# Optimization experiments

Measured on AMD Instinct MI355X. Metric: run time of the kernel, lower is better.

Reference implementation:

```python
import jax, jax.numpy as jnp
import numpy as np

D_MODEL = 1024
N_HEADS = 16
HEAD_DIM = D_MODEL // N_HEADS  # 64
LATENT = 256
B, S = 2, 2048


def setup_inputs() -> dict:
    key = jax.random.key(0)
    ks = jax.random.split(key, 13)
    sc = 0.02
    inp = {
        'x': jax.random.normal(ks[0], (B, S, D_MODEL), jnp.float32),
        'Wq': jax.random.normal(ks[1], (D_MODEL, D_MODEL), jnp.float32) * sc,
        'bq': jnp.zeros((D_MODEL,), jnp.float32),
        'Wkd': jax.random.normal(ks[2], (D_MODEL, LATENT), jnp.float32) * sc,
        'bkd': jnp.zeros((LATENT,), jnp.float32),
        'Wvd': jax.random.normal(ks[3], (D_MODEL, LATENT), jnp.float32) * sc,
        'bvd': jnp.zeros((LATENT,), jnp.float32),
        'Wku': jax.random.normal(ks[4], (LATENT, D_MODEL), jnp.float32) * sc,
        'bku': jnp.zeros((D_MODEL,), jnp.float32),
        'Wvu': jax.random.normal(ks[5], (LATENT, D_MODEL), jnp.float32) * sc,
        'bvu': jnp.zeros((D_MODEL,), jnp.float32),
        'Wo': jax.random.normal(ks[6], (D_MODEL, D_MODEL), jnp.float32) * sc,
        'bo': jnp.zeros((D_MODEL,), jnp.float32),
    }
    return inp


def reference(x, Wq, bq, Wkd, bkd, Wvd, bvd, Wku, bku, Wvu, bvu, Wo, bo):
    b, s, _ = x.shape
    # projections
    Q = x @ Wq + bq                      # [b, s, d_model]
    K_latent = x @ Wkd + bkd             # [b, s, latent]
    V_latent = x @ Wvd + bvd             # [b, s, latent]
    K = K_latent @ Wku + bku             # [b, s, d_model]
    V = V_latent @ Wvu + bvu             # [b, s, d_model]
    # split heads
    Qh = Q.reshape(b, s, N_HEADS, HEAD_DIM)
    Kh = K.reshape(b, s, N_HEADS, HEAD_DIM)
    Vh = V.reshape(b, s, N_HEADS, HEAD_DIM)
    scale = 1.0 / jnp.sqrt(jnp.asarray(HEAD_DIM, x.dtype))
    scores = jnp.einsum('bqhd,bkhd->bhqk', Qh, Kh) * scale  # [b,h,s,s]
    attn = jax.nn.softmax(scores, axis=-1)
    ctx = jnp.einsum('bhqk,bkhd->bqhd', attn, Vh).reshape(b, s, D_MODEL)
    out = ctx @ Wo + bo
    return out
```

## Files before the change

### kernel.cpp

```cpp
#include <hip/hip_runtime.h>
#include <hip/hip_bf16.h>
#include <cstddef>

#define B_SZ 2
#define SEQ  2048
#define DM   1024
#define NH   16
#define HD   64
#define LAT  256
#define MTOT (B_SZ*SEQ)
#define NQKV 1536
#define QSCALE 0.18033688011112042f

typedef short bf16x8 __attribute__((ext_vector_type(8)));
typedef float floatx4 __attribute__((ext_vector_type(4)));
typedef unsigned short u16;

#if __has_builtin(__builtin_amdgcn_exp2f)
#define EXP2(x) __builtin_amdgcn_exp2f(x)
#else
#define EXP2(x) exp2f(x)
#endif

__device__ __forceinline__ u16 f2bf(float f) {
  union { float f; unsigned u; } a; a.f = f;
  unsigned r = a.u + 0x7FFFu + ((a.u >> 16) & 1u);
  return (u16)(r >> 16);
}

__device__ __forceinline__ floatx4 mfma16(bf16x8 a, bf16x8 b, floatx4 c) {
  return __builtin_amdgcn_mfma_f32_16x16x32_bf16(a, b, c, 0, 0, 0);
}

__device__ __forceinline__ void load16(const u16* g, u16* l) {
  __builtin_amdgcn_global_load_lds((const __attribute__((address_space(1))) unsigned*)g,
                                   (__attribute__((address_space(3))) unsigned*)l, 16, 0, 0);
}

__device__ void transpose_tile(const float* __restrict__ W, u16* __restrict__ WT,
                               int K, int N, int k0, int n0, u16 (*t)[65]) {
  const int r = threadIdx.x >> 4;
  const int c4 = (threadIdx.x & 15) * 4;
#pragma unroll
  for (int s = 0; s < 4; s++) {
    int row = s * 16 + r;
    float4 v = *(const float4*)&W[(size_t)(k0 + row) * N + n0 + c4];
    t[row][c4 + 0] = f2bf(v.x); t[row][c4 + 1] = f2bf(v.y);
    t[row][c4 + 2] = f2bf(v.z); t[row][c4 + 3] = f2bf(v.w);
  }
  __syncthreads();
  const int r2 = threadIdx.x >> 2;
  const int c8 = (threadIdx.x & 3) * 16;
  __align__(16) u16 tmp[16];
#pragma unroll
  for (int i = 0; i < 16; i++) tmp[i] = t[c8 + i][r2];
  u16* dst = WT + (size_t)(n0 + r2) * K + k0 + c8;
  *(bf16x8*)dst       = *(const bf16x8*)&tmp[0];
  *(bf16x8*)(dst + 8) = *(const bf16x8*)&tmp[8];
}

__global__ __launch_bounds__(256)
void prep_k(const float* __restrict__ x, u16* __restrict__ xb,
            const float* __restrict__ Wq, const float* __restrict__ Wkd,
            const float* __restrict__ Wvd, const float* __restrict__ Wku,
            const float* __restrict__ Wvu, const float* __restrict__ Wo,
            u16* __restrict__ WstkT, u16* __restrict__ WkuT,
            u16* __restrict__ WvuT, u16* __restrict__ WoT,
            const float* __restrict__ bq, const float* __restrict__ bkd,
            const float* __restrict__ bvd, float* __restrict__ bqkv) {
  __shared__ u16 t[64][65];
  const int blk = blockIdx.x;
  if (blk < 4096) {
    int i = blk * 256 + threadIdx.x;
    float4 v = ((const float4*)x)[i];
    ushort4 o; o.x = f2bf(v.x); o.y = f2bf(v.y); o.z = f2bf(v.z); o.w = f2bf(v.w);
    ((ushort4*)xb)[i] = o;
  } else if (blk < 4352) {
    int tt = blk - 4096;
    transpose_tile(Wq, WstkT, DM, DM, (tt >> 4) * 64, (tt & 15) * 64, t);
  } else if (blk < 4416) {
    int tt = blk - 4352;
    transpose_tile(Wkd, WstkT + (size_t)DM * DM, DM, LAT, (tt >> 2) * 64, (tt & 3) * 64, t);
  } else if (blk < 4480) {
    int tt = blk - 4416;
    transpose_tile(Wvd, WstkT + (size_t)1280 * DM, DM, LAT, (tt >> 2) * 64, (tt & 3) * 64, t);
  } else if (blk < 4544) {
    int tt = blk - 4480;
    transpose_tile(Wku, WkuT, LAT, DM, (tt >> 4) * 64, (tt & 15) * 64, t);
  } else if (blk < 4608) {
    int tt = blk - 4544;
    transpose_tile(Wvu, WvuT, LAT, DM, (tt >> 4) * 64, (tt & 15) * 64, t);
  } else if (blk < 4864) {
    int tt = blk - 4608;
    transpose_tile(Wo, WoT, DM, DM, (tt >> 4) * 64, (tt & 15) * 64, t);
  } else {
    int i = (blk - 4864) * 256 + threadIdx.x;
    float v = (i < 1024) ? bq[i] : (i < 1280) ? bkd[i - 1024] : bvd[i - 1280];
    bqkv[i] = v;
  }
}

template<int TM, int OUT_BF16, int VT1>
__global__ __launch_bounds__(256)
void gemm_bt(const u16* __restrict__ A0, const u16* __restrict__ A1,
             const u16* __restrict__ BT0, const u16* __restrict__ BT1,
             const float* __restrict__ bias0, const float* __restrict__ bias1,
             void* __restrict__ C0, void* __restrict__ C1,
             int M, int N, int Kd, int lda, float qscale, int qcols) {
  constexpr int FM = TM / 32;
  __shared__ u16 As[TM * 64];
  __shared__ u16 Bs[64 * 64];
  const u16* A  = blockIdx.z ? A1 : A0;
  const u16* BT = blockIdx.z ? BT1 : BT0;
  const float* bias = blockIdx.z ? bias1 : bias0;
  void* C = blockIdx.z ? C1 : C0;

  const int tid = threadIdx.x;
  const int m0 = blockIdx.y * TM, n0 = blockIdx.x * 64;
  const int wave = tid >> 6, lane = tid & 63;
  const int l15 = lane & 15, quad = lane >> 4;
  const int wm = (wave >> 1) * (TM / 2), wn = (wave & 1) * 32;

  floatx4 acc[FM][2];
#pragma unroll
  for (int i = 0; i < FM; i++)
#pragma unroll
    for (int j = 0; j < 2; j++) acc[i][j] = (floatx4){0.f, 0.f, 0.f, 0.f};

  const int tr = tid >> 3;
  const int tc8 = (tid & 7) * 8;
  const u16* Ag = A  + (size_t)(m0 + tr) * lda + tc8;
  const u16* Bg = BT + (size_t)(n0 + tr) * Kd + tc8;
  u16* AsW = &As[(size_t)tid * 8];
  u16* BsW = &Bs[(size_t)tid * 8];

  for (int k0 = 0; k0 < Kd; k0 += 64) {
    __syncthreads();
#pragma unroll
    for (int s = 0; s < FM; s++)
      load16(Ag + (size_t)(s * 32) * lda + k0, AsW + s * 2048);
#pragma unroll
    for (int s = 0; s < 2; s++)
      load16(Bg + (size_t)(s * 32) * Kd  + k0, BsW + s * 2048);
    __syncthreads();
#pragma unroll
    for (int kk = 0; kk < 2; kk++) {
      bf16x8 af[FM], bfr[2];
#pragma unroll
      for (int i = 0; i < FM; i++)
        af[i]  = *(const bf16x8*)&As[(wm + i * 16 + l15) * 64 + kk * 32 + quad * 8];
#pragma unroll
      for (int j = 0; j < 2; j++)
        bfr[j] = *(const bf16x8*)&Bs[(wn + j * 16 + l15) * 64 + kk * 32 + quad * 8];
#pragma unroll
      for (int i = 0; i < FM; i++)
#pragma unroll
        for (int j = 0; j < 2; j++)
          acc[i][j] = mfma16(af[i], bfr[j], acc[i][j]);
    }
  }

  if (VT1 && blockIdx.z == 1) {
#pragma unroll
    for (int i = 0; i < FM; i++) {
      int row = m0 + wm + i * 16 + quad * 4;
      int bb = row >> 11, sb = row & 2047;
#pragma unroll
      for (int j = 0; j < 2; j++) {
        int col = n0 + wn + j * 16 + l15;
        float bv = bias[col];
        union { u16 u[4]; uint2 w2; } tv;
#pragma unroll
        for (int r = 0; r < 4; r++) tv.u[r] = f2bf(acc[i][j][r] + bv);
        *(uint2*)((u16*)C + ((size_t)(bb * 16 + (col >> 6)) * 64 + (col & 63)) * SEQ + sb) = tv.w2;
      }
    }
  } else {
#pragma unroll
    for (int i = 0; i < FM; i++) {
      int row = m0 + wm + i * 16 + quad * 4;
#pragma unroll
      for (int j = 0; j < 2; j++) {
        int col = n0 + wn + j * 16 + l15;
        float bv = bias[col];
        float sc = (col < qcols) ? qscale : 1.f;
#pragma unroll
        for (int r = 0; r < 4; r++) {
          float v = (acc[i][j][r] + bv) * sc;
          if (OUT_BF16) ((u16*)C)[(size_t)(row + r) * N + col] = f2bf(v);
          else          ((float*)C)[(size_t)(row + r) * N + col] = v;
        }
      }
    }
  }
}

__global__ __launch_bounds__(256, 2)
void attn_fused(const u16* __restrict__ Q, const u16* __restrict__ K,
                const u16* __restrict__ VT, u16* __restrict__ CTX) {
  __shared__ float Ocmb[64][68];
  __shared__ float Lw[4][64];
  __shared__ u16 Plds[4][64][40];
  const int bh = blockIdx.y, b = bh >> 4, h = bh & 15;
  const int wave = threadIdx.x >> 6, lane = threadIdx.x & 63;
  const int l15 = lane & 15, quad = lane >> 4;
  const int q0 = blockIdx.x * 64;

  bf16x8 qf[4][2];
  {
    const u16* Qp = Q + (size_t)(b * SEQ + q0 + l15) * NQKV + h * HD + quad * 8;
#pragma unroll
    for (int qi = 0; qi < 4; qi++)
#pragma unroll
      for (int h2 = 0; h2 < 2; h2++)
        qf[qi][h2] = *(const bf16x8*)(Qp + (size_t)qi * 16 * NQKV + h2 * 32);
  }
  const u16* Kp = K + (size_t)(b * SEQ) * DM + h * HD + quad * 8;
  const u16* Vp = VT + ((size_t)bh * HD + l15) * SEQ + quad * 8;

  floatx4 o[4][4];
#pragma unroll
  for (int dt = 0; dt < 4; dt++)
#pragma unroll
    for (int qi = 0; qi < 4; qi++) o[dt][qi] = (floatx4){0.f, 0.f, 0.f, 0.f};
  float ls[4] = {0.f, 0.f, 0.f, 0.f};

  const int kb0 = wave * 512;

  bf16x8 kfb[2][2][2], vfb[2][4];
#pragma unroll
  for (int ki = 0; ki < 2; ki++)
#pragma unroll
    for (int h2 = 0; h2 < 2; h2++)
      kfb[0][ki][h2] = *(const bf16x8*)(Kp + (size_t)(kb0 + ki * 16 + l15) * DM + h2 * 32);
#pragma unroll
  for (int dt = 0; dt < 4; dt++)
    vfb[0][dt] = *(const bf16x8*)(Vp + (size_t)(dt * 16) * SEQ + kb0);

#pragma unroll 2
  for (int it = 0; it < 16; ++it) {
    const int cur = it & 1, nxt = cur ^ 1;
    const int kb = kb0 + it * 32;
    if (it < 15) {
      const int kn = kb + 32;
#pragma unroll
      for (int ki = 0; ki < 2; ki++)
#pragma unroll
        for (int h2 = 0; h2 < 2; h2++)
          kfb[nxt][ki][h2] = *(const bf16x8*)(Kp + (size_t)(kn + ki * 16 + l15) * DM + h2 * 32);
#pragma unroll
      for (int dt = 0; dt < 4; dt++)
        vfb[nxt][dt] = *(const bf16x8*)(Vp + (size_t)(dt * 16) * SEQ + kn);
    }
    unsigned pw[4][4];
#pragma unroll
    for (int qi = 0; qi < 4; qi++) {
#pragma unroll
      for (int ki = 0; ki < 2; ki++) {
        floatx4 z = (floatx4){0.f, 0.f, 0.f, 0.f};
        z = mfma16(kfb[cur][ki][0], qf[qi][0], z);
        z = mfma16(kfb[cur][ki][1], qf[qi][1], z);
        float p0 = EXP2(z[0]), p1 = EXP2(z[1]), p2 = EXP2(z[2]), p3 = EXP2(z[3]);
        ls[qi] += (p0 + p1) + (p2 + p3);
        unsigned u0 = __float_as_uint(p0) + 0x8000u;
        unsigned u1 = __float_as_uint(p1) + 0x8000u;
        unsigned u2 = __float_as_uint(p2) + 0x8000u;
        unsigned u3 = __float_as_uint(p3) + 0x8000u;
        pw[qi][ki * 2]     = __builtin_amdgcn_perm(u1, u0, 0x07060302u);
        pw[qi][ki * 2 + 1] = __builtin_amdgcn_perm(u3, u2, 0x07060302u);
      }
    }
#pragma unroll
    for (int qi = 0; qi < 4; qi++) {
      uint2 w0; w0.x = pw[qi][0]; w0.y = pw[qi][1];
      *(uint2*)&Plds[wave][qi * 16 + l15][quad * 4] = w0;
      uint2 w1; w1.x = pw[qi][2]; w1.y = pw[qi][3];
      *(uint2*)&Plds[wave][qi * 16 + l15][16 + quad * 4] = w1;
    }
#pragma unroll
    for (int qi = 0; qi < 4; qi++) {
      bf16x8 pf = *(const bf16x8*)&Plds[wave][qi * 16 + l15][quad * 8];
#pragma unroll
      for (int dt = 0; dt < 4; dt++)
        o[dt][qi] = mfma16(vfb[cur][dt], pf, o[dt][qi]);
    }
  }

#pragma unroll
  for (int qi = 0; qi < 4; qi++) {
    float v = ls[qi];
    v += __shfl_xor(v, 16);
    v += __shfl_xor(v, 32);
    if (quad == 0) Lw[wave][qi * 16 + l15] = v;
  }
  if (wave == 0) {
#pragma unroll
    for (int dt = 0; dt < 4; dt++)
#pragma unroll
      for (int qi = 0; qi < 4; qi++)
        *(floatx4*)&Ocmb[qi * 16 + l15][dt * 16 + quad * 4] = o[dt][qi];
  }
  __syncthreads();
  if (wave == 1) {
#pragma unroll
    for (int dt = 0; dt < 4; dt++)
#pragma unroll
      for (int qi = 0; qi < 4; qi++) {
        floatx4* pp = (floatx4*)&Ocmb[qi * 16 + l15][dt * 16 + quad * 4];
        *pp = *pp + o[dt][qi];
      }
  }
  __syncthreads();
  if (wave == 2) {
#pragma unroll
    for (int dt = 0; dt < 4; dt++)
#pragma unroll
      for (int qi = 0; qi < 4; qi++) {
        floatx4* pp = (floatx4*)&Ocmb[qi * 16 + l15][dt * 16 + quad * 4];
        *pp = *pp + o[dt][qi];
      }
  }
  __syncthreads();
  if (wave == 3) {
#pragma unroll
    for (int qi = 0; qi < 4; qi++) {
      int qq = qi * 16 + l15;
      float lt = Lw[0][qq] + Lw[1][qq] + Lw[2][qq] + Lw[3][qq];
      float inv = 1.f / lt;
      u16* Crow = CTX + (size_t)(b * SEQ + q0 + qq) * DM + h * HD + quad * 4;
#pragma unroll
      for (int dt = 0; dt < 4; dt++) {
        floatx4 ov = o[dt][qi] + *(const floatx4*)&Ocmb[qq][dt * 16 + quad * 4];
        union { u16 u[4]; uint2 w2; } tv;
#pragma unroll
        for (int r = 0; r < 4; r++) tv.u[r] = f2bf(ov[r] * inv);
        *(uint2*)(Crow + dt * 16) = tv.w2;
      }
    }
  }
}

extern "C" void kernel_launch(void* const* d_in, const int* in_sizes, int n_in,
                              void* d_out, int out_size, void* d_ws, size_t ws_size,
                              hipStream_t stream) {
  const float* x   = (const float*)d_in[0];
  const float* Wq  = (const float*)d_in[1];
  const float* bq  = (const float*)d_in[2];
  const float* Wkd = (const float*)d_in[3];
  const float* bkd = (const float*)d_in[4];
  const float* Wvd = (const float*)d_in[5];
  const float* bvd = (const float*)d_in[6];
  const float* Wku = (const float*)d_in[7];
  const float* bku = (const float*)d_in[8];
  const float* Wvu = (const float*)d_in[9];
  const float* bvu = (const float*)d_in[10];
  const float* Wo  = (const float*)d_in[11];
  const float* bo  = (const float*)d_in[12];
  float* out = (float*)d_out;

  float* bqkv = (float*)d_ws;
  u16* p = (u16*)((char*)d_ws + 1536 * sizeof(float));
  u16* xb    = p; p += (size_t)MTOT * DM;
  u16* WstkT = p; p += (size_t)NQKV * DM;
  u16* WkuT  = p; p += (size_t)DM * LAT;
  u16* WvuT  = p; p += (size_t)DM * LAT;
  u16* WoT   = p; p += (size_t)DM * DM;
  u16* QKVb  = p; p += (size_t)MTOT * NQKV;
  u16* Kb    = p; p += (size_t)MTOT * DM;
  u16* VTb   = p; p += (size_t)MTOT * DM;
  u16* CXb   = p; p += (size_t)MTOT * DM;

  prep_k<<<4870, 256, 0, stream>>>(x, xb, Wq, Wkd, Wvd, Wku, Wvu, Wo,
                                   WstkT, WkuT, WvuT, WoT, bq, bkd, bvd, bqkv);

  gemm_bt<128, 1, 0><<<dim3(NQKV / 64, MTOT / 128, 1), 256, 0, stream>>>(
      xb, xb, WstkT, WstkT, bqkv, bqkv, QKVb, QKVb, MTOT, NQKV, DM, DM, QSCALE, DM);
  gemm_bt<128, 1, 1><<<dim3(DM / 64, MTOT / 128, 2), 256, 0, stream>>>(
      QKVb + 1024, QKVb + 1280, WkuT, WvuT, bku, bvu, Kb, VTb, MTOT, DM, LAT, NQKV, 1.f, 0);

  attn_fused<<<dim3(SEQ / 64, B_SZ * NH), 256, 0, stream>>>(QKVb, Kb, VTb, CXb);

  gemm_bt<64, 0, 0><<<dim3(DM / 64, MTOT / 64, 1), 256, 0, stream>>>(
      CXb, CXb, WoT, WoT, bo, bo, out, out, MTOT, DM, DM, DM, 1.f, 0);
}
```

Baseline: 223.3 us.

## Split attention waves 2x2 over query and key halves, drop prefetch buffers

Attention waves now split as two query halves times two key halves. Each wave handles 32 queries over 1024 keys, where before each wave took all 64 queries over 512 keys. The cross-wave reduction shrinks from a three-stage serialized LDS accumulate to one exchange. The register double-buffered K/V prefetch is removed and launch bounds are raised to 3 blocks per CU to gain occupancy instead. The output GEMM also moves to a 128-row tile. Each wave now issues K/V loads per query tile with less reuse and without software prefetch, which may expose memory latency.

```diff
diff --git a/kernel.cpp b/kernel.cpp
--- a/kernel.cpp
+++ b/kernel.cpp
@@ -195,22 +195,23 @@
   }
 }
 
-__global__ __launch_bounds__(256, 2)
+__global__ __launch_bounds__(256, 3)
 void attn_fused(const u16* __restrict__ Q, const u16* __restrict__ K,
                 const u16* __restrict__ VT, u16* __restrict__ CTX) {
-  __shared__ float Ocmb[64][68];
-  __shared__ float Lw[4][64];
-  __shared__ u16 Plds[4][64][40];
+  __shared__ float Ocmb[2][32][68];
+  __shared__ float Lw[2][32];
+  __shared__ u16 Plds[4][32][40];
   const int bh = blockIdx.y, b = bh >> 4, h = bh & 15;
   const int wave = threadIdx.x >> 6, lane = threadIdx.x & 63;
   const int l15 = lane & 15, quad = lane >> 4;
-  const int q0 = blockIdx.x * 64;
-
-  bf16x8 qf[4][2];
+  const int wq = wave & 1, wk = wave >> 1;
+  const int q0 = blockIdx.x * 64 + wq * 32;
+
+  bf16x8 qf[2][2];
   {
     const u16* Qp = Q + (size_t)(b * SEQ + q0 + l15) * NQKV + h * HD + quad * 8;
 #pragma unroll
-    for (int qi = 0; qi < 4; qi++)
+    for (int qi = 0; qi < 2; qi++)
 #pragma unroll
       for (int h2 = 0; h2 < 2; h2++)
         qf[qi][h2] = *(const bf16x8*)(Qp + (size_t)qi * 16 * NQKV + h2 * 32);
@@ -218,48 +219,36 @@
   const u16* Kp = K + (size_t)(b * SEQ) * DM + h * HD + quad * 8;
   const u16* Vp = VT + ((size_t)bh * HD + l15) * SEQ + quad * 8;
 
-  floatx4 o[4][4];
+  floatx4 o[4][2];
 #pragma unroll
   for (int dt = 0; dt < 4; dt++)
 #pragma unroll
-    for (int qi = 0; qi < 4; qi++) o[dt][qi] = (floatx4){0.f, 0.f, 0.f, 0.f};
-  float ls[4] = {0.f, 0.f, 0.f, 0.f};
-
-  const int kb0 = wave * 512;
-
-  bf16x8 kfb[2][2][2], vfb[2][4];
-#pragma unroll
-  for (int ki = 0; ki < 2; ki++)
-#pragma unroll
-    for (int h2 = 0; h2 < 2; h2++)
-      kfb[0][ki][h2] = *(const bf16x8*)(Kp + (size_t)(kb0 + ki * 16 + l15) * DM + h2 * 32);
-#pragma unroll
-  for (int dt = 0; dt < 4; dt++)
-    vfb[0][dt] = *(const bf16x8*)(Vp + (size_t)(dt * 16) * SEQ + kb0);
-
-#pragma unroll 2
-  for (int it = 0; it < 16; ++it) {
-    const int cur = it & 1, nxt = cur ^ 1;
+    for (int qi = 0; qi < 2; qi++) o[dt][qi] = (floatx4){0.f, 0.f, 0.f, 0.f};
+  float ls[2] = {0.f, 0.f};
+
+  const int kb0 = wk * 1024;
+
+  for (int it = 0; it < 32; ++it) {
     const int kb = kb0 + it * 32;
-    if (it < 15) {
-      const int kn = kb + 32;
-#pragma unroll
-      for (int ki = 0; ki < 2; ki++)
-#pragma unroll
-        for (int h2 = 0; h2 < 2; h2++)
-          kfb[nxt][ki][h2] = *(const bf16x8*)(Kp + (size_t)(kn + ki * 16 + l15) * DM + h2 * 32);
-#pragma unroll
-      for (int dt = 0; dt < 4; dt++)
-        vfb[nxt][dt] = *(const bf16x8*)(Vp + (size_t)(dt * 16) * SEQ + kn);
-    }
-    unsigned pw[4][4];
-#pragma unroll
-    for (int qi = 0; qi < 4; qi++) {
+    bf16x8 kf[2][2];
+#pragma unroll
+    for (int ki = 0; ki < 2; ki++)
+#pragma unroll
+      for (int h2 = 0; h2 < 2; h2++)
+        kf[ki][h2] = *(const bf16x8*)(Kp + (size_t)(kb + ki * 16 + l15) * DM + h2 * 32);
+    bf16x8 vf[4];
+#pragma unroll
+    for (int dt = 0; dt < 4; dt++)
+      vf[dt] = *(const bf16x8*)(Vp + (size_t)(dt * 16) * SEQ + kb);
+
+    unsigned pw[2][4];
+#pragma unroll
+    for (int qi = 0; qi < 2; qi++) {
 #pragma unroll
       for (int ki = 0; ki < 2; ki++) {
         floatx4 z = (floatx4){0.f, 0.f, 0.f, 0.f};
-        z = mfma16(kfb[cur][ki][0], qf[qi][0], z);
-        z = mfma16(kfb[cur][ki][1], qf[qi][1], z);
+        z = mfma16(kf[ki][0], qf[qi][0], z);
+        z = mfma16(kf[ki][1], qf[qi][1], z);
         float p0 = EXP2(z[0]), p1 = EXP2(z[1]), p2 = EXP2(z[2]), p3 = EXP2(z[3]);
         ls[qi] += (p0 + p1) + (p2 + p3);
         unsigned u0 = __float_as_uint(p0) + 0x8000u;
@@ -271,66 +260,49 @@
       }
     }
 #pragma unroll
-    for (int qi = 0; qi < 4; qi++) {
+    for (int qi = 0; qi < 2; qi++) {
       uint2 w0; w0.x = pw[qi][0]; w0.y = pw[qi][1];
       *(uint2*)&Plds[wave][qi * 16 + l15][quad * 4] = w0;
       uint2 w1; w1.x = pw[qi][2]; w1.y = pw[qi][3];
       *(uint2*)&Plds[wave][qi * 16 + l15][16 + quad * 4] = w1;
     }
 #pragma unroll
-    for (int qi = 0; qi < 4; qi++) {
+    for (int qi = 0; qi < 2; qi++) {
       bf16x8 pf = *(const bf16x8*)&Plds[wave][qi * 16 + l15][quad * 8];
 #pragma unroll
       for (int dt = 0; dt < 4; dt++)
-        o[dt][qi] = mfma16(vfb[cur][dt], pf, o[dt][qi]);
-    }
-  }
-
-#pragma unroll
-  for (int qi = 0; qi < 4; qi++) {
+        o[dt][qi] = mfma16(vf[dt], pf, o[dt][qi]);
+    }
+  }
+
+  float lfull[2];
+#pragma unroll
+  for (int qi = 0; qi < 2; qi++) {
     float v = ls[qi];
     v += __shfl_xor(v, 16);
     v += __shfl_xor(v, 32);
-    if (quad == 0) Lw[wave][qi * 16 + l15] = v;
-  }
-  if (wave == 0) {
-#pragma unroll
-    for (int dt = 0; dt < 4; dt++)
-#pragma unroll
-      for (int qi = 0; qi < 4; qi++)
-        *(floatx4*)&Ocmb[qi * 16 + l15][dt * 16 + quad * 4] = o[dt][qi];
+    lfull[qi] = v;
+  }
+  if (wk == 0) {
+#pragma unroll
+    for (int qi = 0; qi < 2; qi++) {
+      if (quad == 0) Lw[wq][qi * 16 + l15] = lfull[qi];
+#pragma unroll
+      for (int dt = 0; dt < 4; dt++)
+        *(floatx4*)&Ocmb[wq][qi * 16 + l15][dt * 16 + quad * 4] = o[dt][qi];
+    }
   }
   __syncthreads();
-  if (wave == 1) {
-#pragma unroll
-    for (int dt = 0; dt < 4; dt++)
-#pragma unroll
-      for (int qi = 0; qi < 4; qi++) {
-        floatx4* pp = (floatx4*)&Ocmb[qi * 16 + l15][dt * 16 + quad * 4];
-        *pp = *pp + o[dt][qi];
-      }
-  }
-  __syncthreads();
-  if (wave == 2) {
-#pragma unroll
-    for (int dt = 0; dt < 4; dt++)
-#pragma unroll
-      for (int qi = 0; qi < 4; qi++) {
-        floatx4* pp = (floatx4*)&Ocmb[qi * 16 + l15][dt * 16 + quad * 4];
-        *pp = *pp + o[dt][qi];
-      }
-  }
-  __syncthreads();
-  if (wave == 3) {
-#pragma unroll
-    for (int qi = 0; qi < 4; qi++) {
+  if (wk == 1) {
+#pragma unroll
+    for (int qi = 0; qi < 2; qi++) {
       int qq = qi * 16 + l15;
-      float lt = Lw[0][qq] + Lw[1][qq] + Lw[2][qq] + Lw[3][qq];
+      float lt = Lw[wq][qq] + lfull[qi];
       float inv = 1.f / lt;
       u16* Crow = CTX + (size_t)(b * SEQ + q0 + qq) * DM + h * HD + quad * 4;
 #pragma unroll
       for (int dt = 0; dt < 4; dt++) {
-        floatx4 ov = o[dt][qi] + *(const floatx4*)&Ocmb[qq][dt * 16 + quad * 4];
+        floatx4 ov = o[dt][qi] + *(const floatx4*)&Ocmb[wq][qq][dt * 16 + quad * 4];
         union { u16 u[4]; uint2 w2; } tv;
 #pragma unroll
         for (int r = 0; r < 4; r++) tv.u[r] = f2bf(ov[r] * inv);
@@ -380,6 +352,6 @@
 
   attn_fused<<<dim3(SEQ / 64, B_SZ * NH), 256, 0, stream>>>(QKVb, Kb, VTb, CXb);
 
-  gemm_bt<64, 0, 0><<<dim3(DM / 64, MTOT / 64, 1), 256, 0, stream>>>(
+  gemm_bt<128, 0, 0><<<dim3(DM / 64, MTOT / 128, 1), 256, 0, stream>>>(
       CXb, CXb, WoT, WoT, bo, bo, out, out, MTOT, DM, DM, DM, 1.f, 0);
 }
```

New measurement: 275.6 us. 1.23x slower.

## Use 128x128 GEMM tiles with double-buffered LDS prefetch

Applied to the files above, without the earlier changes.

The GEMM kernel moves from 128x64 (or 64x64) tiles to a fixed 128x128 tile with a 4x4 MFMA fragment grid per wave, and adds a two-stage LDS double buffer so the next K-slice is loaded while the current one is computed. This removes one barrier per iteration and raises arithmetic intensity per loaded byte. The cost is larger register and LDS use (64 KB shared), which lowers occupancy, and fewer blocks: the output projection drops to 256 blocks and the QKV GEMM to 384, which may underfill the GPU's CUs.

```diff
diff --git a/kernel.cpp b/kernel.cpp
--- a/kernel.cpp
+++ b/kernel.cpp
@@ -100,73 +100,78 @@
   }
 }
 
-template<int TM, int OUT_BF16, int VT1>
+template<int OUT_BF16, int VT1>
 __global__ __launch_bounds__(256)
 void gemm_bt(const u16* __restrict__ A0, const u16* __restrict__ A1,
              const u16* __restrict__ BT0, const u16* __restrict__ BT1,
              const float* __restrict__ bias0, const float* __restrict__ bias1,
              void* __restrict__ C0, void* __restrict__ C1,
              int M, int N, int Kd, int lda, float qscale, int qcols) {
-  constexpr int FM = TM / 32;
-  __shared__ u16 As[TM * 64];
-  __shared__ u16 Bs[64 * 64];
+  __shared__ u16 As[2][128 * 64];
+  __shared__ u16 Bs[2][128 * 64];
   const u16* A  = blockIdx.z ? A1 : A0;
   const u16* BT = blockIdx.z ? BT1 : BT0;
   const float* bias = blockIdx.z ? bias1 : bias0;
   void* C = blockIdx.z ? C1 : C0;
 
   const int tid = threadIdx.x;
-  const int m0 = blockIdx.y * TM, n0 = blockIdx.x * 64;
+  const int m0 = blockIdx.y * 128, n0 = blockIdx.x * 128;
   const int wave = tid >> 6, lane = tid & 63;
   const int l15 = lane & 15, quad = lane >> 4;
-  const int wm = (wave >> 1) * (TM / 2), wn = (wave & 1) * 32;
-
-  floatx4 acc[FM][2];
-#pragma unroll
-  for (int i = 0; i < FM; i++)
-#pragma unroll
-    for (int j = 0; j < 2; j++) acc[i][j] = (floatx4){0.f, 0.f, 0.f, 0.f};
+  const int wm = (wave >> 1) * 64, wn = (wave & 1) * 64;
+
+  floatx4 acc[4][4];
+#pragma unroll
+  for (int i = 0; i < 4; i++)
+#pragma unroll
+    for (int j = 0; j < 4; j++) acc[i][j] = (floatx4){0.f, 0.f, 0.f, 0.f};
 
   const int tr = tid >> 3;
   const int tc8 = (tid & 7) * 8;
   const u16* Ag = A  + (size_t)(m0 + tr) * lda + tc8;
   const u16* Bg = BT + (size_t)(n0 + tr) * Kd + tc8;
-  u16* AsW = &As[(size_t)tid * 8];
-  u16* BsW = &Bs[(size_t)tid * 8];
-
-  for (int k0 = 0; k0 < Kd; k0 += 64) {
+
+#pragma unroll
+  for (int s = 0; s < 4; s++) {
+    load16(Ag + (size_t)(s * 32) * lda, &As[0][tid * 8 + s * 2048]);
+    load16(Bg + (size_t)(s * 32) * Kd,  &Bs[0][tid * 8 + s * 2048]);
+  }
+
+  const int NIT = Kd >> 6;
+  for (int it = 0; it < NIT; ++it) {
+    const int cur = it & 1, nxt = cur ^ 1;
     __syncthreads();
-#pragma unroll
-    for (int s = 0; s < FM; s++)
-      load16(Ag + (size_t)(s * 32) * lda + k0, AsW + s * 2048);
-#pragma unroll
-    for (int s = 0; s < 2; s++)
-      load16(Bg + (size_t)(s * 32) * Kd  + k0, BsW + s * 2048);
-    __syncthreads();
+    if (it + 1 < NIT) {
+      const int k0 = (it + 1) * 64;
+#pragma unroll
+      for (int s = 0; s < 4; s++) {
+        load16(Ag + (size_t)(s * 32) * lda + k0, &As[nxt][tid * 8 + s * 2048]);
+        load16(Bg + (size_t)(s * 32) * Kd  + k0, &Bs[nxt][tid * 8 + s * 2048]);
+      }
+    }
 #pragma unroll
     for (int kk = 0; kk < 2; kk++) {
-      bf16x8 af[FM], bfr[2];
-#pragma unroll
-      for (int i = 0; i < FM; i++)
-        af[i]  = *(const bf16x8*)&As[(wm + i * 16 + l15) * 64 + kk * 32 + quad * 8];
-#pragma unroll
-      for (int j = 0; j < 2; j++)
-        bfr[j] = *(const bf16x8*)&Bs[(wn + j * 16 + l15) * 64 + kk * 32 + quad * 8];
-#pragma unroll
-      for (int i = 0; i < FM; i++)
-#pragma unroll
-        for (int j = 0; j < 2; j++)
+      bf16x8 af[4], bfr[4];
+#pragma unroll
+      for (int i = 0; i < 4; i++) {
+        af[i]  = *(const bf16x8*)&As[cur][(wm + i * 16 + l15) * 64 + kk * 32 + quad * 8];
+        bfr[i] = *(const bf16x8*)&Bs[cur][(wn + i * 16 + l15) * 64 + kk * 32 + quad * 8];
+      }
+#pragma unroll
+      for (int i = 0; i < 4; i++)
+#pragma unroll
+        for (int j = 0; j < 4; j++)
           acc[i][j] = mfma16(af[i], bfr[j], acc[i][j]);
     }
   }
 
   if (VT1 && blockIdx.z == 1) {
 #pragma unroll
-    for (int i = 0; i < FM; i++) {
+    for (int i = 0; i < 4; i++) {
       int row = m0 + wm + i * 16 + quad * 4;
       int bb = row >> 11, sb = row & 2047;
 #pragma unroll
-      for (int j = 0; j < 2; j++) {
+      for (int j = 0; j < 4; j++) {
         int col = n0 + wn + j * 16 + l15;
         float bv = bias[col];
         union { u16 u[4]; uint2 w2; } tv;
@@ -177,10 +182,10 @@
     }
   } else {
 #pragma unroll
-    for (int i = 0; i < FM; i++) {
+    for (int i = 0; i < 4; i++) {
       int row = m0 + wm + i * 16 + quad * 4;
 #pragma unroll
-      for (int j = 0; j < 2; j++) {
+      for (int j = 0; j < 4; j++) {
         int col = n0 + wn + j * 16 + l15;
         float bv = bias[col];
         float sc = (col < qcols) ? qscale : 1.f;
@@ -373,13 +378,13 @@
   prep_k<<<4870, 256, 0, stream>>>(x, xb, Wq, Wkd, Wvd, Wku, Wvu, Wo,
                                    WstkT, WkuT, WvuT, WoT, bq, bkd, bvd, bqkv);
 
-  gemm_bt<128, 1, 0><<<dim3(NQKV / 64, MTOT / 128, 1), 256, 0, stream>>>(
+  gemm_bt<1, 0><<<dim3(NQKV / 128, MTOT / 128, 1), 256, 0, stream>>>(
       xb, xb, WstkT, WstkT, bqkv, bqkv, QKVb, QKVb, MTOT, NQKV, DM, DM, QSCALE, DM);
-  gemm_bt<128, 1, 1><<<dim3(DM / 64, MTOT / 128, 2), 256, 0, stream>>>(
+  gemm_bt<1, 1><<<dim3(DM / 128, MTOT / 128, 2), 256, 0, stream>>>(
       QKVb + 1024, QKVb + 1280, WkuT, WvuT, bku, bvu, Kb, VTb, MTOT, DM, LAT, NQKV, 1.f, 0);
 
   attn_fused<<<dim3(SEQ / 64, B_SZ * NH), 256, 0, stream>>>(QKVb, Kb, VTb, CXb);
 
-  gemm_bt<64, 0, 0><<<dim3(DM / 64, MTOT / 64, 1), 256, 0, stream>>>(
+  gemm_bt<0, 0><<<dim3(DM / 128, MTOT / 128, 1), 256, 0, stream>>>(
       CXb, CXb, WoT, WoT, bo, bo, out, out, MTOT, DM, DM, DM, 1.f, 0);
 }
```

New measurement: 230.7 us. 3.3% more time.
